# Optimization experiments

Hardware: AMD Instinct MI355X
Metric: run time of the kernel (lower is better)

## Reference

```python
import jax, jax.numpy as jnp
import numpy as np

SEQ_LEN, BATCH, HID, EMB, VOCAB = 80, 5120, 256, 8, 100


def lstm_layer(xs, w_ih, w_hh, b_ih, b_hh):
    # xs: [T, B, in]; PyTorch gate order i, f, g, o
    B = xs.shape[1]
    H = w_hh.shape[1]
    x_proj = jnp.einsum('tbi,gi->tbg', xs, w_ih) + b_ih + b_hh  # [T, B, 4H]

    def step(carry, xp_t):
        h, c = carry
        gates = xp_t + h @ w_hh.T
        i, f, g, o = jnp.split(gates, 4, axis=-1)
        c = jax.nn.sigmoid(f) * c + jax.nn.sigmoid(i) * jnp.tanh(g)
        h = jax.nn.sigmoid(o) * jnp.tanh(c)
        return (h, c), h

    init = (jnp.zeros((B, H), xs.dtype), jnp.zeros((B, H), xs.dtype))
    (h_n, c_n), ys = jax.lax.scan(step, init, x_proj)
    return ys, h_n


def setup_inputs() -> dict:
    key = jax.random.key(0)
    ks = jax.random.split(key, 12)
    s_h = 1.0 / np.sqrt(HID)
    inp = {
        'x': jax.random.randint(ks[0], (SEQ_LEN, BATCH), 0, VOCAB),
        'emb': jax.random.normal(ks[1], (VOCAB, EMB), jnp.float32),
        'w_ih0': jax.random.uniform(ks[2], (4 * HID, EMB), jnp.float32, -s_h, s_h),
        'w_hh0': jax.random.uniform(ks[3], (4 * HID, HID), jnp.float32, -s_h, s_h),
        'b_ih0': jax.random.uniform(ks[4], (4 * HID,), jnp.float32, -s_h, s_h),
        'b_hh0': jax.random.uniform(ks[5], (4 * HID,), jnp.float32, -s_h, s_h),
        'w_ih1': jax.random.uniform(ks[6], (4 * HID, HID), jnp.float32, -s_h, s_h),
        'w_hh1': jax.random.uniform(ks[7], (4 * HID, HID), jnp.float32, -s_h, s_h),
        'b_ih1': jax.random.uniform(ks[8], (4 * HID,), jnp.float32, -s_h, s_h),
        'b_hh1': jax.random.uniform(ks[9], (4 * HID,), jnp.float32, -s_h, s_h),
        'dec_w': jax.random.uniform(ks[10], (VOCAB, HID * SEQ_LEN), jnp.float32, -0.01, 0.01),
        'dec_b': jax.random.uniform(ks[11], (VOCAB,), jnp.float32, -0.01, 0.01),
    }
    return inp


def reference(x, emb, w_ih0, w_hh0, b_ih0, b_hh0, w_ih1, w_hh1, b_ih1, b_hh1, dec_w, dec_b):
    encoded = emb[x]                                   # [T, B, EMB]
    ys0, _ = lstm_layer(encoded, w_ih0, w_hh0, b_ih0, b_hh0)  # [T, B, H]
    ys1, _ = lstm_layer(ys0, w_ih1, w_hh1, b_ih1, b_hh1)      # [T, B, H]
    last = ys1[-1]                                     # [B, H] (last timestep)
    # faithful to original quirk: view(-1, hidden*seq_len) -> [B/seq_len, H*T]
    flat = last.reshape(-1, HID * SEQ_LEN)
    return flat @ dec_w.T + dec_b                      # [B/seq_len, VOCAB]
```

## Files before the change

kernel.cpp:

```cpp
#include <hip/hip_runtime.h>

#define T_SEQ 80
#define NB    5120
#define NBH   (NB * 256)
#define NVOC  100

#define OFF_TABLE0 0u
#define OFF_BIAS1  409600u
#define OFF_BPACK  413696u
#define OFF_RING0  1986560u
#define OFF_RING1  7229440u
#define OFF_C0     12472320u
#define OFF_C1     15093760u

#define SMEM_BYTES 42624

typedef float  f32x4  __attribute__((ext_vector_type(4)));
typedef __bf16 bf16x8 __attribute__((ext_vector_type(8)));
typedef short  s16x8  __attribute__((ext_vector_type(8)));
typedef _Float16 f16x4 __attribute__((ext_vector_type(4)));
typedef unsigned short u16x8 __attribute__((ext_vector_type(8)));

__device__ __forceinline__ int colmap(int np) {
  int gate = (np >> 4) & 3;
  int j    = ((np >> 6) << 4) | (np & 15);
  return gate * 256 + j;
}

__device__ __forceinline__ unsigned short f2bf(float f) {
  unsigned int u = __float_as_uint(f);
  u += 0x7fffu + ((u >> 16) & 1u);
  return (unsigned short)(u >> 16);
}
__device__ __forceinline__ float bf2f(unsigned short s) {
  return __uint_as_float(((unsigned int)s) << 16);
}
__device__ __forceinline__ float sigm(float x) {
  x = fminf(fmaxf(x, -20.f), 20.f);
  return 1.f / (1.f + __expf(-x));
}
__device__ __forceinline__ float tanh_(float x) {
  x = fminf(fmaxf(x, -10.f), 10.f);
  float e = __expf(2.f * x);
  return (e - 1.f) / (e + 1.f);
}

__global__ void prep_kernel(const float* __restrict__ emb,
                            const float* __restrict__ w_ih0, const float* __restrict__ w_hh0,
                            const float* __restrict__ b_ih0, const float* __restrict__ b_hh0,
                            const float* __restrict__ w_ih1, const float* __restrict__ w_hh1,
                            const float* __restrict__ b_ih1, const float* __restrict__ b_hh1,
                            float* __restrict__ table0, float* __restrict__ bias1,
                            unsigned short* __restrict__ Bpack) {
  int idx = blockIdx.x * 256 + threadIdx.x;
  if (idx < 102400) {
    int v = idx >> 10, np = idx & 1023;
    int row = colmap(np);
    float s = b_ih0[row] + b_hh0[row];
#pragma unroll
    for (int e = 0; e < 8; ++e) s = fmaf(emb[v * 8 + e], w_ih0[row * 8 + e], s);
    table0[idx] = s;
  } else if (idx < 103424) {
    int np = idx - 102400;
    bias1[np] = b_ih1[colmap(np)] + b_hh1[colmap(np)];
  } else {
    int i2 = idx - 103424;
    int i    = i2 & 7;
    int t    = (i2 >> 3) & 511;
    int ni   = (i2 >> 12) & 7;
    int slot = i2 >> 15;
    int np   = ni * 128 + ((t >> 6) << 4) + (t & 15);
    int row  = colmap(np);
    int k    = (((t & 63) >> 4) << 3) + i;
    float val;
    if (slot < 8) {
      val = w_hh0[row * 256 + slot * 32 + k];
    } else {
      int kc = slot - 8;
      const float* W = (kc < 8) ? w_ih1 : w_hh1;
      val = W[row * 256 + (kc & 7) * 32 + k];
    }
    Bpack[i2] = f2bf(val);
  }
}

__global__ __launch_bounds__(256, 1) void step_kernel(
    int s, const int* __restrict__ x,
    const float* __restrict__ table0, const float* __restrict__ bias1,
    const unsigned short* __restrict__ Bpack,
    unsigned short* __restrict__ ring0, unsigned short* __restrict__ ring1,
    _Float16* __restrict__ c0h, _Float16* __restrict__ c1h) {
  extern __shared__ char smem[];
  char* Ab = smem;
  char* Bb = smem + 25600;
  int*  xs = (int*)(smem + 41984);

  const int tid = threadIdx.x;
  const int lane = tid & 63, wid = tid >> 6;
  const int l15 = lane & 15, lhi = lane >> 4;
  const int wm = wid >> 1, wn = wid & 1, rw = wm * 80;

  const int p = blockIdx.x;
  const int xcd = p & 7, idx = p >> 3;
  const bool isL0 = idx < 32;
  const int sub = idx & 31;
  const int mi = xcd * 4 + (sub >> 3);
  const int ni = sub & 7;
  const int rows = mi * 160;

  int t;
  if (isL0) { if (s == T_SEQ) return; t = s; }
  else      { if (s == 0)     return; t = s - 1; }

  const unsigned short* ring0Prev = ring0 + ((s + 1) & 1) * NBH;
  unsigned short*       ring0Cur  = ring0 + (s & 1) * NBH;
  const unsigned short* h1Prev    = ring1 + (s & 1) * NBH;
  unsigned short*       h1Cur     = ring1 + ((s + 1) & 1) * NBH;

  const int KC = isL0 ? (t > 0 ? 8 : 0) : (t > 0 ? 16 : 8);

  if (isL0 && tid < 160) xs[tid] = x[t * NB + rows + tid];

  f32x4 acc[5][4];
#pragma unroll
  for (int m = 0; m < 5; ++m)
#pragma unroll
    for (int nf = 0; nf < 4; ++nf) acc[m][nf] = (f32x4)0.f;

  uint4 au0, au1, au2;
  s16x8 bsr0, bsr1;

#define LOADR(kc_) do { \
    const unsigned short* _As; int _ko; \
    if (isL0) { _As = ring0Prev; _ko = (kc_) * 32; } \
    else { _As = ((kc_) < 8) ? ring0Prev : h1Prev; _ko = ((kc_) & 7) * 32; } \
    { int _c = tid;       au0 = *(const uint4*)(_As + (rows + (_c >> 2)) * 256 + _ko + ((_c & 3) << 3)); } \
    { int _c = tid + 256; au1 = *(const uint4*)(_As + (rows + (_c >> 2)) * 256 + _ko + ((_c & 3) << 3)); } \
    if (tid < 128) { int _c = tid + 512; au2 = *(const uint4*)(_As + (rows + (_c >> 2)) * 256 + _ko + ((_c & 3) << 3)); } \
    int _slot = isL0 ? (kc_) : (8 + (kc_)); \
    bsr0 = *(const s16x8*)(Bpack + (((_slot * 8 + ni) * 512 + tid) << 3)); \
    bsr1 = *(const s16x8*)(Bpack + (((_slot * 8 + ni) * 512 + tid + 256) << 3)); \
  } while (0)

#define STORER(buf_) do { \
    char* _ab = Ab + (buf_) * 12800; \
    *(uint4*)(_ab + (tid >> 2) * 80 + (tid & 3) * 16) = au0; \
    { int _c = tid + 256; *(uint4*)(_ab + (_c >> 2) * 80 + (_c & 3) * 16) = au1; } \
    if (tid < 128) { int _c = tid + 512; *(uint4*)(_ab + (_c >> 2) * 80 + (_c & 3) * 16) = au2; } \
    char* _bb = Bb + (buf_) * 8192; \
    *(s16x8*)(_bb + tid * 16) = bsr0; \
    *(s16x8*)(_bb + (tid + 256) * 16) = bsr1; \
  } while (0)

#define CONSUME(buf_) do { \
    const char* _ab = Ab + (buf_) * 12800; \
    const char* _bp = Bb + (buf_) * 8192; \
    bf16x8 _bld[4]; \
    _Pragma("unroll") \
    for (int _nf = 0; _nf < 4; ++_nf) \
      _bld[_nf] = *(const bf16x8*)(_bp + ((wn * 4 + _nf) * 64 + lane) * 16); \
    _Pragma("unroll") \
    for (int _m = 0; _m < 5; ++_m) { \
      bf16x8 _a = *(const bf16x8*)(_ab + (rw + _m * 16 + l15) * 80 + lhi * 16); \
      _Pragma("unroll") \
      for (int _nf = 0; _nf < 4; ++_nf) \
        acc[_m][_nf] = __builtin_amdgcn_mfma_f32_16x16x32_bf16(_a, _bld[_nf], acc[_m][_nf], 0, 0, 0); \
    } \
  } while (0)

  if (KC > 0) { LOADR(0); STORER(0); }
#pragma unroll 1
  for (int kc = 0; kc < KC; ++kc) {
    __syncthreads();
    const bool more = (kc + 1 < KC);
    if (more) LOADR(kc + 1);
    CONSUME(kc & 1);
    if (more) STORER((kc + 1) & 1);
  }
  if (KC == 0) __syncthreads();

  const int jh = (ni * 2 + wn) * 16 + l15;
  if (isL0) {
    const int tbb = ni * 128 + wn * 64 + l15;
#pragma unroll
    for (int m = 0; m < 5; ++m) {
      const int cbase = ((rows + rw + m * 16) >> 2) + lhi;
      f16x4 cold4 = (f16x4)(_Float16)0.f;
      if (t > 0) cold4 = *(const f16x4*)(c0h + cbase * 1024 + jh * 4);
      f16x4 cnew;
#pragma unroll
      for (int r = 0; r < 4; ++r) {
        int rowl = rw + m * 16 + lhi * 4 + r;
        const float* tb = table0 + xs[rowl] * 1024 + tbb;
        float gi = acc[m][0][r] + tb[0];
        float gf = acc[m][1][r] + tb[16];
        float gg = acc[m][2][r] + tb[32];
        float go = acc[m][3][r] + tb[48];
        float cn = sigm(gf) * (float)cold4[r] + sigm(gi) * tanh_(gg);
        cnew[r] = (_Float16)cn;
        ring0Cur[(rows + rowl) * 256 + jh] = f2bf(sigm(go) * tanh_(cn));
      }
      *(f16x4*)(c0h + cbase * 1024 + jh * 4) = cnew;
    }
  } else {
    const int bbb = ni * 128 + wn * 64 + l15;
    float b0 = bias1[bbb], b1 = bias1[bbb + 16], b2 = bias1[bbb + 32], b3 = bias1[bbb + 48];
#pragma unroll
    for (int m = 0; m < 5; ++m) {
      const int cbase = ((rows + rw + m * 16) >> 2) + lhi;
      f16x4 cold4 = (f16x4)(_Float16)0.f;
      if (t > 0) cold4 = *(const f16x4*)(c1h + cbase * 1024 + jh * 4);
      f16x4 cnew;
#pragma unroll
      for (int r = 0; r < 4; ++r) {
        int rowl = rw + m * 16 + lhi * 4 + r;
        float gi = acc[m][0][r] + b0;
        float gf = acc[m][1][r] + b1;
        float gg = acc[m][2][r] + b2;
        float go = acc[m][3][r] + b3;
        float cn = sigm(gf) * (float)cold4[r] + sigm(gi) * tanh_(gg);
        cnew[r] = (_Float16)cn;
        h1Cur[(rows + rowl) * 256 + jh] = f2bf(sigm(go) * tanh_(cn));
      }
      *(f16x4*)(c1h + cbase * 1024 + jh * 4) = cnew;
    }
  }
#undef LOADR
#undef STORER
#undef CONSUME
}

__global__ __launch_bounds__(256) void decoder_kernel(
    const unsigned short* __restrict__ h1, const float* __restrict__ dec_w,
    const float* __restrict__ dec_b, float* __restrict__ out) {
  __shared__ float hs[5120];
  const int tid = threadIdx.x, lane = tid & 63, wid = tid >> 6;
  const int b = blockIdx.x;
  const int r = b >> 2;
  const int qoff = (b & 3) * 5120;

  const unsigned short* src = h1 + (size_t)b * 5120;
  for (int i = tid; i < 640; i += 256) {
    u16x8 v8 = *(const u16x8*)(src + i * 8);
#pragma unroll
    for (int e = 0; e < 8; ++e) hs[i * 8 + e] = bf2f(v8[e]);
  }
  __syncthreads();

  for (int vv = wid; vv < NVOC; vv += 4) {
    const float* wp = dec_w + (size_t)vv * 20480 + qoff + lane * 4;
    const float* hp = hs + lane * 4;
    float s = 0.f;
#pragma unroll
    for (int it = 0; it < 20; ++it) {
      f32x4 w4 = *(const f32x4*)(wp + it * 256);
      f32x4 h4 = *(const f32x4*)(hp + it * 256);
      s += w4[0] * h4[0] + w4[1] * h4[1] + w4[2] * h4[2] + w4[3] * h4[3];
    }
#pragma unroll
    for (int off = 32; off > 0; off >>= 1) s += __shfl_down(s, off, 64);
    if (lane == 0) {
      if ((b & 3) == 0) s += dec_b[vv];
      atomicAdd(&out[r * 100 + vv], s);
    }
  }
}

extern "C" void kernel_launch(void* const* d_in, const int* in_sizes, int n_in,
                              void* d_out, int out_size, void* d_ws, size_t ws_size,
                              hipStream_t stream) {
  const int*   x     = (const int*)d_in[0];
  const float* emb   = (const float*)d_in[1];
  const float* w_ih0 = (const float*)d_in[2];
  const float* w_hh0 = (const float*)d_in[3];
  const float* b_ih0 = (const float*)d_in[4];
  const float* b_hh0 = (const float*)d_in[5];
  const float* w_ih1 = (const float*)d_in[6];
  const float* w_hh1 = (const float*)d_in[7];
  const float* b_ih1 = (const float*)d_in[8];
  const float* b_hh1 = (const float*)d_in[9];
  const float* dec_w = (const float*)d_in[10];
  const float* dec_b = (const float*)d_in[11];
  float* out = (float*)d_out;
  char* ws = (char*)d_ws;

  float*          table0 = (float*)(ws + OFF_TABLE0);
  float*          bias1  = (float*)(ws + OFF_BIAS1);
  unsigned short* Bpack  = (unsigned short*)(ws + OFF_BPACK);
  unsigned short* ring0  = (unsigned short*)(ws + OFF_RING0);
  unsigned short* ring1  = (unsigned short*)(ws + OFF_RING1);
  _Float16*       c0h    = (_Float16*)(ws + OFF_C0);
  _Float16*       c1h    = (_Float16*)(ws + OFF_C1);

  hipMemsetAsync(out, 0, (size_t)out_size * 4, stream);
  prep_kernel<<<3476, 256, 0, stream>>>(emb, w_ih0, w_hh0, b_ih0, b_hh0,
                                        w_ih1, w_hh1, b_ih1, b_hh1,
                                        table0, bias1, Bpack);
  hipFuncSetAttribute((const void*)step_kernel,
                      hipFuncAttributeMaxDynamicSharedMemorySize, SMEM_BYTES);
  for (int s = 0; s <= T_SEQ; ++s)
    step_kernel<<<512, 256, SMEM_BYTES, stream>>>(s, x, table0, bias1, Bpack,
                                                  ring0, ring1, c0h, c1h);
  decoder_kernel<<<256, 256, 0, stream>>>(ring1 + NBH, dec_w, dec_b, out);
}
```

Before: 1.523 ms.

## Triple-buffer K-chunk pipeline in LSTM step kernel and split decoder finer

The step kernel moves from a double-buffered shared-memory pipeline to three buffers, with two register stages (A/B) holding the next two K-chunks in flight. Each global load now has about two MFMA consume phases to cover its latency instead of one. The cost is more shared memory and more registers per thread. Separately, the decoder is split into 512 blocks, each handling half as much of the reduction, which doubles the atomic adds into the output.

```diff
diff --git a/kernel.cpp b/kernel.cpp
--- a/kernel.cpp
+++ b/kernel.cpp
@@ -13,7 +13,7 @@
 #define OFF_C0     12472320u
 #define OFF_C1     15093760u
 
-#define SMEM_BYTES 42624
+#define SMEM_BYTES 63616
 
 typedef float  f32x4  __attribute__((ext_vector_type(4)));
 typedef __bf16 bf16x8 __attribute__((ext_vector_type(8)));
@@ -92,8 +92,8 @@
     _Float16* __restrict__ c0h, _Float16* __restrict__ c1h) {
   extern __shared__ char smem[];
   char* Ab = smem;
-  char* Bb = smem + 25600;
-  int*  xs = (int*)(smem + 41984);
+  char* Bb = smem + 38400;
+  int*  xs = (int*)(smem + 62976);
 
   const int tid = threadIdx.x;
   const int lane = tid & 63, wid = tid >> 6;
@@ -127,34 +127,34 @@
 #pragma unroll
     for (int nf = 0; nf < 4; ++nf) acc[m][nf] = (f32x4)0.f;
 
-  uint4 au0, au1, au2;
-  s16x8 bsr0, bsr1;
-
-#define LOADR(kc_) do { \
+  uint4 auA0, auA1, auA2, auB0, auB1, auB2;
+  s16x8 bsA0, bsA1, bsB0, bsB1;
+
+#define LOADR(S, kc_) do { \
     const unsigned short* _As; int _ko; \
     if (isL0) { _As = ring0Prev; _ko = (kc_) * 32; } \
     else { _As = ((kc_) < 8) ? ring0Prev : h1Prev; _ko = ((kc_) & 7) * 32; } \
-    { int _c = tid;       au0 = *(const uint4*)(_As + (rows + (_c >> 2)) * 256 + _ko + ((_c & 3) << 3)); } \
-    { int _c = tid + 256; au1 = *(const uint4*)(_As + (rows + (_c >> 2)) * 256 + _ko + ((_c & 3) << 3)); } \
-    if (tid < 128) { int _c = tid + 512; au2 = *(const uint4*)(_As + (rows + (_c >> 2)) * 256 + _ko + ((_c & 3) << 3)); } \
+    { int _c = tid;       au##S##0 = *(const uint4*)(_As + (rows + (_c >> 2)) * 256 + _ko + ((_c & 3) << 3)); } \
+    { int _c = tid + 256; au##S##1 = *(const uint4*)(_As + (rows + (_c >> 2)) * 256 + _ko + ((_c & 3) << 3)); } \
+    if (tid < 128) { int _c = tid + 512; au##S##2 = *(const uint4*)(_As + (rows + (_c >> 2)) * 256 + _ko + ((_c & 3) << 3)); } \
     int _slot = isL0 ? (kc_) : (8 + (kc_)); \
-    bsr0 = *(const s16x8*)(Bpack + (((_slot * 8 + ni) * 512 + tid) << 3)); \
-    bsr1 = *(const s16x8*)(Bpack + (((_slot * 8 + ni) * 512 + tid + 256) << 3)); \
+    bs##S##0 = *(const s16x8*)(Bpack + (((_slot * 8 + ni) * 512 + tid) << 3)); \
+    bs##S##1 = *(const s16x8*)(Bpack + (((_slot * 8 + ni) * 512 + tid + 256) << 3)); \
   } while (0)
 
-#define STORER(buf_) do { \
-    char* _ab = Ab + (buf_) * 12800; \
-    *(uint4*)(_ab + (tid >> 2) * 80 + (tid & 3) * 16) = au0; \
-    { int _c = tid + 256; *(uint4*)(_ab + (_c >> 2) * 80 + (_c & 3) * 16) = au1; } \
-    if (tid < 128) { int _c = tid + 512; *(uint4*)(_ab + (_c >> 2) * 80 + (_c & 3) * 16) = au2; } \
-    char* _bb = Bb + (buf_) * 8192; \
-    *(s16x8*)(_bb + tid * 16) = bsr0; \
-    *(s16x8*)(_bb + (tid + 256) * 16) = bsr1; \
+#define STORER(S, ob_) do { \
+    char* _ab = Ab + (ob_) * 12800; \
+    *(uint4*)(_ab + (tid >> 2) * 80 + (tid & 3) * 16) = au##S##0; \
+    { int _c = tid + 256; *(uint4*)(_ab + (_c >> 2) * 80 + (_c & 3) * 16) = au##S##1; } \
+    if (tid < 128) { int _c = tid + 512; *(uint4*)(_ab + (_c >> 2) * 80 + (_c & 3) * 16) = au##S##2; } \
+    char* _bb = Bb + (ob_) * 8192; \
+    *(s16x8*)(_bb + tid * 16) = bs##S##0; \
+    *(s16x8*)(_bb + (tid + 256) * 16) = bs##S##1; \
   } while (0)
 
-#define CONSUME(buf_) do { \
-    const char* _ab = Ab + (buf_) * 12800; \
-    const char* _bp = Bb + (buf_) * 8192; \
+#define CONSUME(ob_) do { \
+    const char* _ab = Ab + (ob_) * 12800; \
+    const char* _bp = Bb + (ob_) * 8192; \
     bf16x8 _bld[4]; \
     _Pragma("unroll") \
     for (int _nf = 0; _nf < 4; ++_nf) \
@@ -168,16 +168,27 @@
     } \
   } while (0)
 
-  if (KC > 0) { LOADR(0); STORER(0); }
+  if (KC > 0) {
+    LOADR(A, 0);
+    LOADR(B, 1);
+    STORER(A, 0);
+    int bufc = 0;
 #pragma unroll 1
-  for (int kc = 0; kc < KC; ++kc) {
+    for (int kc = 0; kc < KC; kc += 2) {
+      const int b1 = (bufc + 1) % 3, b2 = (bufc + 2) % 3;
+      __syncthreads();
+      if (kc + 2 < KC) LOADR(A, kc + 2);
+      CONSUME(bufc);
+      STORER(B, b1);
+      __syncthreads();
+      if (kc + 3 < KC) LOADR(B, kc + 3);
+      CONSUME(b1);
+      if (kc + 2 < KC) STORER(A, b2);
+      bufc = b2;
+    }
+  } else {
     __syncthreads();
-    const bool more = (kc + 1 < KC);
-    if (more) LOADR(kc + 1);
-    CONSUME(kc & 1);
-    if (more) STORER((kc + 1) & 1);
-  }
-  if (KC == 0) __syncthreads();
+  }
 
   const int jh = (ni * 2 + wn) * 16 + l15;
   if (isL0) {
@@ -233,14 +244,14 @@
 __global__ __launch_bounds__(256) void decoder_kernel(
     const unsigned short* __restrict__ h1, const float* __restrict__ dec_w,
     const float* __restrict__ dec_b, float* __restrict__ out) {
-  __shared__ float hs[5120];
+  __shared__ float hs[2560];
   const int tid = threadIdx.x, lane = tid & 63, wid = tid >> 6;
   const int b = blockIdx.x;
-  const int r = b >> 2;
-  const int qoff = (b & 3) * 5120;
-
-  const unsigned short* src = h1 + (size_t)b * 5120;
-  for (int i = tid; i < 640; i += 256) {
+  const int r = b >> 3;
+  const int qoff = (b & 7) * 2560;
+
+  const unsigned short* src = h1 + (size_t)b * 2560;
+  for (int i = tid; i < 320; i += 256) {
     u16x8 v8 = *(const u16x8*)(src + i * 8);
 #pragma unroll
     for (int e = 0; e < 8; ++e) hs[i * 8 + e] = bf2f(v8[e]);
@@ -252,7 +263,7 @@
     const float* hp = hs + lane * 4;
     float s = 0.f;
 #pragma unroll
-    for (int it = 0; it < 20; ++it) {
+    for (int it = 0; it < 10; ++it) {
       f32x4 w4 = *(const f32x4*)(wp + it * 256);
       f32x4 h4 = *(const f32x4*)(hp + it * 256);
       s += w4[0] * h4[0] + w4[1] * h4[1] + w4[2] * h4[2] + w4[3] * h4[3];
@@ -260,7 +271,7 @@
 #pragma unroll
     for (int off = 32; off > 0; off >>= 1) s += __shfl_down(s, off, 64);
     if (lane == 0) {
-      if ((b & 3) == 0) s += dec_b[vv];
+      if ((b & 7) == 0) s += dec_b[vv];
       atomicAdd(&out[r * 100 + vv], s);
     }
   }
@@ -301,5 +312,5 @@
   for (int s = 0; s <= T_SEQ; ++s)
     step_kernel<<<512, 256, SMEM_BYTES, stream>>>(s, x, table0, bias1, Bpack,
                                                   ring0, ring1, c0h, c1h);
-  decoder_kernel<<<256, 256, 0, stream>>>(ring1 + NBH, dec_w, dec_b, out);
-}
+  decoder_kernel<<<512, 256, 0, stream>>>(ring1 + NBH, dec_w, dec_b, out);
+}
```

Result: slower. 1.648 ms (+8.3%).
